# Kernel optimization log

Measured on AMD Instinct MI355X. Metric: run time of the kernel, lower is better.

The kernel has to match this reference:

```python
import jax, jax.numpy as jnp
import numpy as np
from jax.scipy.special import logsumexp

T, B, D, L = 1024, 32, 768, 48
NEG = jnp.float32(-1e20)


def setup_inputs() -> dict:
    key = jax.random.key(0)
    ks = jax.random.split(key, 10)
    feats = jax.random.normal(ks[0], (T, B, D), jnp.float32)
    # tags: True = label disallowed at this position (partial annotation mask)
    tags = jax.random.uniform(ks[1], (T, B, L)) < 0.3
    lens = jax.random.randint(ks[2], (B,), T // 2, T + 1)
    W = jax.random.normal(ks[3], (D, L), jnp.float32) * 0.02
    b = jnp.zeros((L,), jnp.float32)
    base = jnp.float32(1.0 / L)
    begin_transition = jnp.full((L,), base) + 0.01 * jax.random.normal(ks[4], (L,), jnp.float32)
    transitions = jnp.full((L, L), base) + 0.01 * jax.random.normal(ks[5], (L, L), jnp.float32)
    end_transition = jnp.full((L,), base) + 0.01 * jax.random.normal(ks[6], (L,), jnp.float32)
    begin_constraints = jax.random.uniform(ks[7], (L,)) < 0.2
    end_constraints = jax.random.uniform(ks[8], (L,)) < 0.2
    transition_constraints = jax.random.uniform(ks[9], (L, L)) < 0.2
    return {
        "feats": feats, "tags": tags, "lens": lens,
        "W": W, "b": b,
        "begin_transition": begin_transition, "transitions": transitions,
        "end_transition": end_transition,
        "begin_constraints": begin_constraints, "end_constraints": end_constraints,
        "transition_constraints": transition_constraints,
    }


def _crf_logZ(emissions, begin, trans, end, tag_mask, lens):
    """Forward algorithm over [T,B,L] emissions; tag_mask True = disallowed.
    Returns log partition per batch element, read out at step lens-1."""
    fs0 = emissions[0] + begin[None, :]              # [B, L]
    fs0 = jnp.where(tag_mask[0], NEG, fs0)

    def step(prev, xs):
        em_t, m_t = xs
        # new[b, j] = logsumexp_k(prev[b, k] + trans[j, k]) + em_t[b, j]
        new = logsumexp(prev[:, None, :] + trans[None, :, :], axis=-1) + em_t
        new = jnp.where(m_t, NEG, new)
        return new, new

    _, ys = jax.lax.scan(step, fs0, (emissions[1:], tag_mask[1:]))
    all_fs = jnp.concatenate([fs0[None], ys], axis=0)        # [T, B, L]
    last = all_fs[lens - 1, jnp.arange(lens.shape[0])]       # [B, L]
    return logsumexp(last + end[None, :], axis=-1)           # [B]


def reference(feats, tags, lens, W, b, begin_transition, transitions,
              end_transition, begin_constraints, end_constraints,
              transition_constraints):
    # feature2labels (Dropout is identity in eval)
    emissions = jnp.einsum('tbd,dl->tbl', feats, W) + b      # [T, B, L]
    no_mask = jnp.zeros_like(tags)

    # forward_alg: unconstrained partition function
    fwd = _crf_logZ(emissions, begin_transition, transitions,
                    end_transition, no_mask, lens)

    # partial_score: constrained params + gold tag masking
    begin_m = jnp.where(begin_constraints, NEG, begin_transition)
    trans_m = jnp.where(transition_constraints, NEG, transitions)
    end_m = jnp.where(end_constraints, NEG, end_transition)
    par = _crf_logZ(emissions, begin_m, trans_m, end_m, tags, lens)

    # criterion per batch element (sum over batch = original scalar loss)
    return fwd - par                                          # [B]
```

## Files before the change

### kernel.cpp

```cpp
#include <hip/hip_runtime.h>

#define T_ 1024
#define B_ 32
#define D_ 768
#define L_ 48
#define TB_ (T_ * B_)

typedef __attribute__((ext_vector_type(4))) float f32x4;

__global__ __launch_bounds__(256, 1) void emis_gemm(
    const float* __restrict__ feats, const float* __restrict__ W,
    const float* __restrict__ bias, float* __restrict__ E) {
  __shared__ float fbuf[2][128 * 64];
  __shared__ float wbuf[2][48 * 68];
  const int tid = threadIdx.x;
  const int wv = tid >> 6;
  const int lane = tid & 63;
  const int cg = tid & 7;
  const int rg = tid >> 3;
  const int c0 = cg * 6;
  const int rowbase = blockIdx.x * 128;
  const int r7 = rg & 7;
  const int r_in = lane >> 4;
  const int slot = lane & 15;

  int woff[12];
#pragma unroll
  for (int i = 0; i < 12; i++) {
    const int idx = tid + i * 256;
    const int ko = idx / 48;
    const int j = idx - ko * 48;
    woff[i] = j * 68 + ko;
  }

  float acc[4][6];
#pragma unroll
  for (int i = 0; i < 4; i++)
#pragma unroll
    for (int c = 0; c < 6; c++) acc[i][c] = 0.f;

  float wr[12];

  {
#pragma unroll
    for (int i = 0; i < 12; i++) wr[i] = W[tid + i * 256];
#pragma unroll
    for (int inst = 0; inst < 8; inst++) {
      const int rowstart = wv * 32 + inst * 4;
      const int r = rowstart + r_in;
      const int gch = slot ^ (r & 7);
      const float* g = feats + (size_t)(rowbase + r) * D_ + gch * 4;
      float* l = &fbuf[0][rowstart * 64];
      __builtin_amdgcn_global_load_lds(
          (const __attribute__((address_space(1))) uint32_t*)g,
          (__attribute__((address_space(3))) uint32_t*)l, 16, 0, 0);
    }
#pragma unroll
    for (int i = 0; i < 12; i++) wbuf[0][woff[i]] = wr[i];
  }

  for (int c = 0; c < 12; c++) {
    const int cur = c & 1;
    __syncthreads();

    if (c < 11) {
      const int kc2 = (c + 1) * 64;
#pragma unroll
      for (int i = 0; i < 12; i++) wr[i] = W[kc2 * L_ + tid + i * 256];
#pragma unroll
      for (int inst = 0; inst < 8; inst++) {
        const int rowstart = wv * 32 + inst * 4;
        const int r = rowstart + r_in;
        const int gch = slot ^ (r & 7);
        const float* g = feats + (size_t)(rowbase + r) * D_ + kc2 + gch * 4;
        float* l = &fbuf[cur ^ 1][rowstart * 64];
        __builtin_amdgcn_global_load_lds(
            (const __attribute__((address_space(1))) uint32_t*)g,
            (__attribute__((address_space(3))) uint32_t*)l, 16, 0, 0);
      }
    }

    const float* fb = fbuf[cur];
    const float* wb = wbuf[cur];
#pragma unroll 4
    for (int k4 = 0; k4 < 16; k4++) {
      float4 fv[4];
      float4 wv4[6];
      const int sch = (k4 ^ r7) << 2;
#pragma unroll
      for (int i = 0; i < 4; i++)
        fv[i] = *(const float4*)(fb + (rg + 32 * i) * 64 + sch);
#pragma unroll
      for (int cc = 0; cc < 6; cc++)
        wv4[cc] = *(const float4*)(wb + (c0 + cc) * 68 + k4 * 4);
#pragma unroll
      for (int i = 0; i < 4; i++) {
#pragma unroll
        for (int cc = 0; cc < 6; cc++) {
          acc[i][cc] = fmaf(fv[i].x, wv4[cc].x, acc[i][cc]);
          acc[i][cc] = fmaf(fv[i].y, wv4[cc].y, acc[i][cc]);
          acc[i][cc] = fmaf(fv[i].z, wv4[cc].z, acc[i][cc]);
          acc[i][cc] = fmaf(fv[i].w, wv4[cc].w, acc[i][cc]);
        }
      }
    }

    if (c < 11) {
#pragma unroll
      for (int i = 0; i < 12; i++) wbuf[cur ^ 1][woff[i]] = wr[i];
    }
  }

#pragma unroll
  for (int i = 0; i < 4; i++) {
    float* dst = E + (size_t)(rowbase + rg + 32 * i) * L_ + c0;
#pragma unroll
    for (int cc = 0; cc < 6; cc += 2) {
      float2 v;
      v.x = __expf(acc[i][cc + 0] + bias[c0 + cc + 0]);
      v.y = __expf(acc[i][cc + 1] + bias[c0 + cc + 1]);
      *(float2*)(dst + cc) = v;
    }
  }
}

__global__ __launch_bounds__(128, 1) void crf_scan(
    const float* __restrict__ E, const int* __restrict__ tags,
    const int* __restrict__ lens, const float* __restrict__ begin,
    const float* __restrict__ trans, const float* __restrict__ endt,
    const int* __restrict__ bc, const int* __restrict__ ec,
    const int* __restrict__ tc, float* __restrict__ out) {
  __shared__ __align__(16) float sbuf[2][2][64];
  __shared__ float lzbuf[2];
  const int b = blockIdx.x;
  const int wv = threadIdx.x >> 6;
  const int lane = threadIdx.x & 63;
  const bool act = lane < L_;
  const bool par = (wv == 1);
  const int len = lens[b];
  const int stride = B_ * L_;
  const int base = b * L_ + (act ? lane : 0);

  float P[L_];
#pragma unroll
  for (int k = 0; k < L_; k++) P[k] = 0.f;
  if (act) {
#pragma unroll
    for (int k = 0; k < L_; k++) {
      float v = __expf(trans[lane * L_ + k]);
      if (par && tc[lane * L_ + k]) v = 0.f;
      P[k] = v;
    }
  }

  float a = 0.f;
  if (act) {
    a = E[base] * __expf(begin[lane]);
    if (par && (bc[lane] || tags[base])) a = 0.f;
  }
  float logacc = 0.f;

  sbuf[wv][0][lane] = a;

  auto step = [&](int i, float ev, int tg, bool resc) {
    const f32x4* src = (const f32x4*)sbuf[wv][i & 1];
    float s0 = 0.f, s1 = 0.f, s2 = 0.f, s3 = 0.f;
    f32x4 mx = {0.f, 0.f, 0.f, 0.f};
#pragma unroll
    for (int c = 0; c < 12; c++) {
      const f32x4 q = src[c];
      if (resc) {
        mx.x = fmaxf(mx.x, q.x);
        mx.y = fmaxf(mx.y, q.y);
        mx.z = fmaxf(mx.z, q.z);
        mx.w = fmaxf(mx.w, q.w);
      }
      s0 = fmaf(q.x, P[4 * c + 0], s0);
      s1 = fmaf(q.y, P[4 * c + 1], s1);
      s2 = fmaf(q.z, P[4 * c + 2], s2);
      s3 = fmaf(q.w, P[4 * c + 3], s3);
    }
    float evp = ev;
    if (resc) {
      float m = fmaxf(fmaxf(mx.x, mx.y), fmaxf(mx.z, mx.w));
      m = fmaxf(m, 1e-30f);
      logacc += __logf(m);
      evp = ev * (1.f / m);
    }
    float u = ((s0 + s1) + (s2 + s3)) * evp;
    if (tg) u = 0.f;
    a = u;
    sbuf[wv][(i + 1) & 1][lane] = u;
  };

  float e4[4];
  int tg4[4];
#pragma unroll
  for (int i = 0; i < 4; i++) {
    e4[i] = E[(size_t)(1 + i) * stride + base];
    tg4[i] = par ? tags[(size_t)(1 + i) * stride + base] : 0;
  }

  int t = 1;
  for (; t + 4 <= len; t += 4) {
    float p4[4];
    int q4[4];
#pragma unroll
    for (int i = 0; i < 4; i++) {
      int tt = t + 4 + i;
      tt = (tt < len) ? tt : (len - 1);
      p4[i] = E[(size_t)tt * stride + base];
      q4[i] = par ? tags[(size_t)tt * stride + base] : 0;
    }
    if ((t & 7) == 1) {
      step(0, e4[0], tg4[0], true);
    } else {
      step(0, e4[0], tg4[0], false);
    }
    step(1, e4[1], tg4[1], false);
    step(2, e4[2], tg4[2], false);
    step(3, e4[3], tg4[3], false);
#pragma unroll
    for (int i = 0; i < 4; i++) { e4[i] = p4[i]; tg4[i] = q4[i]; }
  }
#pragma unroll
  for (int i = 0; i < 4; i++) {
    if (t + i < len) step(i, e4[i], tg4[i], false);
  }

  float z = 0.f;
  if (act) {
    float ez = __expf(endt[lane]);
    if (par && ec[lane]) ez = 0.f;
    z = a * ez;
  }
#pragma unroll
  for (int off = 32; off; off >>= 1) z += __shfl_xor(z, off, 64);
  if (lane == 0) lzbuf[wv] = logacc + __logf(z);
  __syncthreads();
  if (threadIdx.x == 0) out[b] = lzbuf[0] - lzbuf[1];
}

extern "C" void kernel_launch(void* const* d_in, const int* in_sizes, int n_in,
                              void* d_out, int out_size, void* d_ws,
                              size_t ws_size, hipStream_t stream) {
  (void)in_sizes; (void)n_in; (void)out_size; (void)ws_size;
  const float* feats = (const float*)d_in[0];
  const int* tags = (const int*)d_in[1];
  const int* lens = (const int*)d_in[2];
  const float* W = (const float*)d_in[3];
  const float* bias = (const float*)d_in[4];
  const float* begin = (const float*)d_in[5];
  const float* trans = (const float*)d_in[6];
  const float* endt = (const float*)d_in[7];
  const int* bc = (const int*)d_in[8];
  const int* ec = (const int*)d_in[9];
  const int* tc = (const int*)d_in[10];

  float* E = (float*)d_ws;
  float* out = (float*)d_out;

  emis_gemm<<<dim3(TB_ / 128), dim3(256), 0, stream>>>(feats, W, bias, E);
  crf_scan<<<dim3(B_), dim3(128), 0, stream>>>(E, tags, lens, begin, trans,
                                               endt, bc, ec, tc, out);
}
```

Baseline: 446.7 us.

## Shrink GEMM tile to single-buffered 64 rows and move CRF transition matrix to LDS

The emission GEMM now uses 64-row tiles with a single LDS buffer and no register-staged prefetch of W. It launches twice as many blocks and allows two blocks per CU, aiming for better occupancy and lower register and LDS pressure. The CRF scan no longer keeps the 48 transition weights in registers: it stores them in padded LDS rows and reloads them as float4 on every step, which frees registers. The cost is the lost overlap between global loads and compute in the GEMM, plus extra LDS reads inside the latency-bound serial recurrence.

```diff
diff --git a/kernel.cpp b/kernel.cpp
--- a/kernel.cpp
+++ b/kernel.cpp
@@ -8,93 +8,66 @@
 
 typedef __attribute__((ext_vector_type(4))) float f32x4;
 
-__global__ __launch_bounds__(256, 1) void emis_gemm(
+__global__ __launch_bounds__(256, 2) void emis_gemm(
     const float* __restrict__ feats, const float* __restrict__ W,
     const float* __restrict__ bias, float* __restrict__ E) {
-  __shared__ float fbuf[2][128 * 64];
-  __shared__ float wbuf[2][48 * 68];
+  __shared__ float fbuf[64 * 64];
+  __shared__ float wbuf[48 * 68];
   const int tid = threadIdx.x;
   const int wv = tid >> 6;
   const int lane = tid & 63;
   const int cg = tid & 7;
   const int rg = tid >> 3;
   const int c0 = cg * 6;
-  const int rowbase = blockIdx.x * 128;
+  const int rowbase = blockIdx.x * 64;
   const int r7 = rg & 7;
   const int r_in = lane >> 4;
   const int slot = lane & 15;
 
-  int woff[12];
-#pragma unroll
-  for (int i = 0; i < 12; i++) {
-    const int idx = tid + i * 256;
-    const int ko = idx / 48;
-    const int j = idx - ko * 48;
-    woff[i] = j * 68 + ko;
-  }
-
-  float acc[4][6];
-#pragma unroll
-  for (int i = 0; i < 4; i++)
+  float acc[2][6];
+#pragma unroll
+  for (int i = 0; i < 2; i++)
 #pragma unroll
     for (int c = 0; c < 6; c++) acc[i][c] = 0.f;
 
-  float wr[12];
-
-  {
-#pragma unroll
-    for (int i = 0; i < 12; i++) wr[i] = W[tid + i * 256];
-#pragma unroll
-    for (int inst = 0; inst < 8; inst++) {
-      const int rowstart = wv * 32 + inst * 4;
+  for (int kc = 0; kc < D_; kc += 64) {
+    __syncthreads();
+
+#pragma unroll
+    for (int inst = 0; inst < 4; inst++) {
+      const int rowstart = wv * 16 + inst * 4;
       const int r = rowstart + r_in;
       const int gch = slot ^ (r & 7);
-      const float* g = feats + (size_t)(rowbase + r) * D_ + gch * 4;
-      float* l = &fbuf[0][rowstart * 64];
+      const float* g = feats + (size_t)(rowbase + r) * D_ + kc + gch * 4;
+      float* l = fbuf + rowstart * 64;
       __builtin_amdgcn_global_load_lds(
           (const __attribute__((address_space(1))) uint32_t*)g,
           (__attribute__((address_space(3))) uint32_t*)l, 16, 0, 0);
     }
-#pragma unroll
-    for (int i = 0; i < 12; i++) wbuf[0][woff[i]] = wr[i];
-  }
-
-  for (int c = 0; c < 12; c++) {
-    const int cur = c & 1;
+
+#pragma unroll
+    for (int i = 0; i < 12; i++) {
+      const int idx = tid + i * 256;
+      const int ko = idx / 48;
+      const int j = idx - ko * 48;
+      wbuf[j * 68 + ko] = W[(kc + ko) * L_ + j];
+    }
+
     __syncthreads();
 
-    if (c < 11) {
-      const int kc2 = (c + 1) * 64;
-#pragma unroll
-      for (int i = 0; i < 12; i++) wr[i] = W[kc2 * L_ + tid + i * 256];
-#pragma unroll
-      for (int inst = 0; inst < 8; inst++) {
-        const int rowstart = wv * 32 + inst * 4;
-        const int r = rowstart + r_in;
-        const int gch = slot ^ (r & 7);
-        const float* g = feats + (size_t)(rowbase + r) * D_ + kc2 + gch * 4;
-        float* l = &fbuf[cur ^ 1][rowstart * 64];
-        __builtin_amdgcn_global_load_lds(
-            (const __attribute__((address_space(1))) uint32_t*)g,
-            (__attribute__((address_space(3))) uint32_t*)l, 16, 0, 0);
-      }
-    }
-
-    const float* fb = fbuf[cur];
-    const float* wb = wbuf[cur];
 #pragma unroll 4
     for (int k4 = 0; k4 < 16; k4++) {
-      float4 fv[4];
+      float4 fv[2];
       float4 wv4[6];
       const int sch = (k4 ^ r7) << 2;
 #pragma unroll
-      for (int i = 0; i < 4; i++)
-        fv[i] = *(const float4*)(fb + (rg + 32 * i) * 64 + sch);
+      for (int i = 0; i < 2; i++)
+        fv[i] = *(const float4*)(fbuf + (rg + 32 * i) * 64 + sch);
 #pragma unroll
       for (int cc = 0; cc < 6; cc++)
-        wv4[cc] = *(const float4*)(wb + (c0 + cc) * 68 + k4 * 4);
-#pragma unroll
-      for (int i = 0; i < 4; i++) {
+        wv4[cc] = *(const float4*)(wbuf + (c0 + cc) * 68 + k4 * 4);
+#pragma unroll
+      for (int i = 0; i < 2; i++) {
 #pragma unroll
         for (int cc = 0; cc < 6; cc++) {
           acc[i][cc] = fmaf(fv[i].x, wv4[cc].x, acc[i][cc]);
@@ -104,15 +77,10 @@
         }
       }
     }
-
-    if (c < 11) {
-#pragma unroll
-      for (int i = 0; i < 12; i++) wbuf[cur ^ 1][woff[i]] = wr[i];
-    }
-  }
-
-#pragma unroll
-  for (int i = 0; i < 4; i++) {
+  }
+
+#pragma unroll
+  for (int i = 0; i < 2; i++) {
     float* dst = E + (size_t)(rowbase + rg + 32 * i) * L_ + c0;
 #pragma unroll
     for (int cc = 0; cc < 6; cc += 2) {
@@ -124,13 +92,14 @@
   }
 }
 
-__global__ __launch_bounds__(128, 1) void crf_scan(
+__global__ __launch_bounds__(128) void crf_scan(
     const float* __restrict__ E, const int* __restrict__ tags,
     const int* __restrict__ lens, const float* __restrict__ begin,
     const float* __restrict__ trans, const float* __restrict__ endt,
     const int* __restrict__ bc, const int* __restrict__ ec,
     const int* __restrict__ tc, float* __restrict__ out) {
   __shared__ __align__(16) float sbuf[2][2][64];
+  __shared__ __align__(16) float pbuf[2][48 * 52];
   __shared__ float lzbuf[2];
   const int b = blockIdx.x;
   const int wv = threadIdx.x >> 6;
@@ -141,17 +110,15 @@
   const int stride = B_ * L_;
   const int base = b * L_ + (act ? lane : 0);
 
-  float P[L_];
-#pragma unroll
-  for (int k = 0; k < L_; k++) P[k] = 0.f;
   if (act) {
 #pragma unroll
     for (int k = 0; k < L_; k++) {
       float v = __expf(trans[lane * L_ + k]);
       if (par && tc[lane * L_ + k]) v = 0.f;
-      P[k] = v;
-    }
-  }
+      pbuf[wv][lane * 52 + k] = v;
+    }
+  }
+  const f32x4* prow = (const f32x4*)(pbuf[wv] + (act ? lane : 0) * 52);
 
   float a = 0.f;
   if (act) {
@@ -168,6 +135,7 @@
     f32x4 mx = {0.f, 0.f, 0.f, 0.f};
 #pragma unroll
     for (int c = 0; c < 12; c++) {
+      const f32x4 pq = prow[c];
       const f32x4 q = src[c];
       if (resc) {
         mx.x = fmaxf(mx.x, q.x);
@@ -175,10 +143,10 @@
         mx.z = fmaxf(mx.z, q.z);
         mx.w = fmaxf(mx.w, q.w);
       }
-      s0 = fmaf(q.x, P[4 * c + 0], s0);
-      s1 = fmaf(q.y, P[4 * c + 1], s1);
-      s2 = fmaf(q.z, P[4 * c + 2], s2);
-      s3 = fmaf(q.w, P[4 * c + 3], s3);
+      s0 = fmaf(q.x, pq.x, s0);
+      s1 = fmaf(q.y, pq.y, s1);
+      s2 = fmaf(q.z, pq.z, s2);
+      s3 = fmaf(q.w, pq.w, s3);
     }
     float evp = ev;
     if (resc) {
@@ -260,7 +228,7 @@
   float* E = (float*)d_ws;
   float* out = (float*)d_out;
 
-  emis_gemm<<<dim3(TB_ / 128), dim3(256), 0, stream>>>(feats, W, bias, E);
+  emis_gemm<<<dim3(TB_ / 64), dim3(256), 0, stream>>>(feats, W, bias, E);
   crf_scan<<<dim3(B_), dim3(128), 0, stream>>>(E, tags, lens, begin, trans,
                                                endt, bc, ec, tc, out);
 }
```

Result: slower. 462.4 us (+3.5%).
